# Kernel optimization log

Measured on AMD Instinct MI355X. Metric: run time of the kernel, lower is better.

## Reference

```python
import jax, jax.numpy as jnp
import numpy as np

EMBED_DIM = 768
NUM_HEADS = 12
HEAD_DIM = EMBED_DIM // NUM_HEADS
BSZ = 8
N_NODE = 512


def setup_inputs() -> dict:
    key = jax.random.key(0)
    ks = jax.random.split(key, 12)
    s = 0.02
    E = EMBED_DIM
    return {
        "query": jax.random.normal(ks[0], (N_NODE, BSZ, E), jnp.float32),
        "attention_bias": jax.random.normal(ks[1], (BSZ, NUM_HEADS, N_NODE, N_NODE), jnp.float32),
        "node_position": jax.random.normal(ks[2], (BSZ, N_NODE, 3), jnp.float32),
        "Wq": jax.random.normal(ks[3], (E, E), jnp.float32) * s,
        "bq": jnp.zeros((E,), jnp.float32),
        "Wk": jax.random.normal(ks[4], (E, E), jnp.float32) * s,
        "bk": jnp.zeros((E,), jnp.float32),
        "Wv": jax.random.normal(ks[5], (E, E), jnp.float32) * s,
        "bv": jnp.zeros((E,), jnp.float32),
        "W1": jax.random.normal(ks[6], (E, 1), jnp.float32) * s,
        "b1": jnp.zeros((1,), jnp.float32),
        "W2": jax.random.normal(ks[7], (E, 1), jnp.float32) * s,
        "b2": jnp.zeros((1,), jnp.float32),
        "W3": jax.random.normal(ks[8], (E, 1), jnp.float32) * s,
        "b3": jnp.zeros((1,), jnp.float32),
    }


def reference(query, attention_bias, node_position, Wq, bq, Wk, bk, Wv, bv,
              W1, b1, W2, b2, W3, b3):
    bsz, n = node_position.shape[:2]
    H = attention_bias.shape[1]
    E = query.shape[-1]
    hd = E // H
    scaling = hd ** -0.5

    # unit direction vectors between node pairs: delta[b,i,j] = pos[j]-pos[i]
    delta = node_position[:, None, :, :] - node_position[:, :, None, :]  # (b,n,n,3)
    dist = jnp.linalg.norm(delta, axis=-1)                               # (b,n,n)
    delta = delta / (dist[..., None] + 1e-5)

    x = jnp.swapaxes(query, 0, 1)  # (b,n,E)
    q = (x @ Wq + bq).reshape(bsz, n, H, hd).transpose(0, 2, 1, 3) * scaling  # (b,h,n,d)
    k = (x @ Wk + bk).reshape(bsz, n, H, hd).transpose(0, 2, 1, 3)
    v = (x @ Wv + bv).reshape(bsz, n, H, hd).transpose(0, 2, 1, 3)

    attn = jnp.einsum('bhid,bhjd->bhij', q, k)
    probs = jax.nn.softmax(attn + attention_bias, axis=-1)  # (b,h,i,j); dropout = identity (eval)

    # rotational aggregation: out[b,i,c,h,d] = sum_j probs[b,h,i,j]*delta[b,i,j,c]*v[b,h,j,d]
    xo = jnp.einsum('bhij,bijc,bhjd->bichd', probs, delta, v).reshape(bsz, n, 3, E)

    f1 = xo[:, :, 0, :] @ W1 + b1  # (b,n,1)
    f2 = xo[:, :, 1, :] @ W2 + b2
    f3 = xo[:, :, 2, :] @ W3 + b3
    return jnp.concatenate([f1, f2, f3], axis=-1).astype(jnp.float32)  # (b,n,3)
```

## Files before the change

kernel.cpp:

```cpp
#include <hip/hip_runtime.h>
#include <math.h>

#define EDIM 768
#define NH 12
#define HD 64
#define BSZ 8
#define NN 512
#define NCAT 1664

typedef short short8 __attribute__((ext_vector_type(8)));
typedef float f32x4 __attribute__((ext_vector_type(4)));

__device__ __forceinline__ unsigned short f2bf(float x) {
    unsigned int u = __float_as_uint(x);
    u = (u + 0x7FFF + ((u >> 16) & 1)) >> 16;
    return (unsigned short)u;
}
__device__ __forceinline__ void gl2lds16(const void* g, void* l) {
    __builtin_amdgcn_global_load_lds(
        (const __attribute__((address_space(1))) unsigned int*)g,
        (__attribute__((address_space(3))) unsigned int*)l, 16, 0, 0);
}

#define PB_TR_END   1152
#define PB_VW_END   1260
#define PB_CVT_END  2028
#define PB_BC_END   2035
#define PREP_BLOCKS 2070

__global__ __launch_bounds__(256) void k_prep(
        const float* __restrict__ query,
        const float* __restrict__ Wq, const float* __restrict__ bq,
        const float* __restrict__ Wk, const float* __restrict__ bk,
        const float* __restrict__ Wv, const float* __restrict__ bv,
        const float* __restrict__ W1, const float* __restrict__ W2,
        const float* __restrict__ W3,
        unsigned short* __restrict__ WT, float* __restrict__ bcat,
        unsigned short* __restrict__ Xb) {
    __shared__ float sm[1536];
    const int bid = blockIdx.x;
    const int t = threadIdx.x;

    if (bid < PB_TR_END) {
        float (*tile)[33] = (float(*)[33])sm;
        const int n0 = (bid % 48) * 32, e0 = (bid / 48) * 32;
        const float* src = (n0 < 768) ? Wq : Wk;
        const float sc = (n0 < 768) ? 0.125f : 1.0f;
        const int ol0 = (n0 < 768) ? n0 : (n0 - 768);
        const int tx = t & 31, ty = t >> 5;
        #pragma unroll
        for (int s = 0; s < 4; s++)
            tile[ty + s * 8][tx] = src[(size_t)(e0 + ty + s * 8) * EDIM + ol0 + tx];
        __syncthreads();
        #pragma unroll
        for (int s = 0; s < 4; s++)
            WT[(size_t)(n0 + ty + s * 8) * EDIM + e0 + tx] = f2bf(tile[tx][ty + s * 8] * sc);
    } else if (bid < PB_VW_END) {
        int idx = (bid - PB_TR_END) * 256 + t;
        int o2 = idx / 768, e = idx - o2 * 768;
        int h = o2 / 3, c = o2 - (o2 / 3) * 3;
        const float* Wc = (c == 0) ? W1 : (c == 1) ? W2 : W3;
        const float4* wvp = (const float4*)(Wv + (size_t)e * EDIM + h * HD);
        const float4* wcp = (const float4*)(Wc + h * HD);
        float s = 0.f;
        #pragma unroll
        for (int d4 = 0; d4 < 16; d4++) {
            float4 a = wvp[d4], b = wcp[d4];
            s += a.x * b.x + a.y * b.y + a.z * b.z + a.w * b.w;
        }
        WT[(size_t)(1536 + o2) * EDIM + e] = f2bf(s);
    } else if (bid < PB_CVT_END) {
        int base = (bid - PB_VW_END) * 256 + t;
        #pragma unroll
        for (int half = 0; half < 2; half++) {
            int idx = base + half * 196608;
            int m = idx / 96, e8 = (idx - (idx / 96) * 96) * 8;
            int b = m >> 9, i = m & (NN - 1);
            const float* src = query + ((size_t)i * BSZ + b) * EDIM + e8;
            float4 v0 = *(const float4*)src;
            float4 v1 = *(const float4*)(src + 4);
            unsigned int p0 = f2bf(v0.x) | ((unsigned int)f2bf(v0.y) << 16);
            unsigned int p1 = f2bf(v0.z) | ((unsigned int)f2bf(v0.w) << 16);
            unsigned int p2 = f2bf(v1.x) | ((unsigned int)f2bf(v1.y) << 16);
            unsigned int p3 = f2bf(v1.z) | ((unsigned int)f2bf(v1.w) << 16);
            uint4 pk = {p0, p1, p2, p3};
            *(uint4*)&Xb[(size_t)idx * 8] = pk;
        }
    } else if (bid < PB_BC_END) {
        int o = (bid - PB_CVT_END) * 256 + t;
        if (o < NCAT) {
            float v = 0.f;
            if (o < 768) v = bq[o] * 0.125f;
            else if (o < 1536) v = bk[o - 768];
            else if (o < 1572) {
                int o2 = o - 1536;
                int h = o2 / 3, c = o2 - (o2 / 3) * 3;
                const float* Wc = (c == 0) ? W1 : (c == 1) ? W2 : W3;
                float s = 0.f;
                for (int d = 0; d < HD; d++) s += bv[h * HD + d] * Wc[h * HD + d];
                v = s;
            }
            bcat[o] = v;
        }
    } else {
        int tid = (bid - PB_BC_END) * 256 + t;
        if (tid < 8832) {
            uint4 z = {0, 0, 0, 0};
            *(uint4*)&WT[(size_t)1572 * EDIM + (size_t)tid * 8] = z;
        }
    }
}

__global__ __launch_bounds__(256) void k_gemm_qkv(
        const unsigned short* __restrict__ Xb, const unsigned short* __restrict__ WT,
        const float* __restrict__ bcat,
        unsigned short* __restrict__ qb, unsigned short* __restrict__ kb,
        float* __restrict__ vwb) {
    __shared__ short As[8 * 128 * 8];
    __shared__ short Bs[8 * 128 * 8];
    const int t = threadIdx.x;
    const int m0 = blockIdx.x * 128, n0 = blockIdx.y * 128;
    const int w = t >> 6, lane = t & 63, quad = lane >> 4, ln = lane & 15;
    const int wr = (w & 1) * 64, wc = (w >> 1) * 64;

    f32x4 acc[4][4];
    #pragma unroll
    for (int mi = 0; mi < 4; mi++)
        #pragma unroll
        for (int ni = 0; ni < 4; ni++) acc[mi][ni] = (f32x4){0.f, 0.f, 0.f, 0.f};

    for (int k0 = 0; k0 < EDIM; k0 += 64) {
        __syncthreads();
        #pragma unroll
        for (int is = 0; is < 4; is++) {
            int slot = is * 256 + t;
            int g = slot >> 7, m = slot & 127;
            gl2lds16(Xb + (size_t)(m0 + m) * EDIM + k0 + g * 8, &As[(size_t)(is * 256 + w * 64) * 8]);
        }
        #pragma unroll
        for (int is = 0; is < 4; is++) {
            int slot = is * 256 + t;
            int g = slot >> 7, n = slot & 127;
            gl2lds16(WT + (size_t)(n0 + n) * EDIM + k0 + g * 8, &Bs[(size_t)(is * 256 + w * 64) * 8]);
        }
        __syncthreads();
        #pragma unroll
        for (int s = 0; s < 2; s++) {
            short8 af[4], bf[4];
            #pragma unroll
            for (int mi = 0; mi < 4; mi++)
                af[mi] = *(const short8*)&As[(size_t)((s * 4 + quad) * 128 + wr + mi * 16 + ln) * 8];
            #pragma unroll
            for (int ni = 0; ni < 4; ni++)
                bf[ni] = *(const short8*)&Bs[(size_t)((s * 4 + quad) * 128 + wc + ni * 16 + ln) * 8];
            #pragma unroll
            for (int mi = 0; mi < 4; mi++)
                #pragma unroll
                for (int ni = 0; ni < 4; ni++)
                    acc[mi][ni] = __builtin_amdgcn_mfma_f32_16x16x32_bf16(af[mi], bf[ni], acc[mi][ni], 0, 0, 0);
        }
    }

    #pragma unroll
    for (int mi = 0; mi < 4; mi++) {
        #pragma unroll
        for (int r = 0; r < 4; r++) {
            int mg = m0 + wr + mi * 16 + quad * 4 + r;
            int b_ = mg >> 9, i_ = mg & (NN - 1);
            #pragma unroll
            for (int ni = 0; ni < 4; ni++) {
                int o = n0 + wc + ni * 16 + ln;
                float val = acc[mi][ni][r] + bcat[o];
                if (o < 768) {
                    int h = o >> 6, d = o & 63;
                    qb[(((size_t)b_ * NH + h) * NN + i_) * HD + d] = f2bf(val);
                } else if (o < 1536) {
                    int o2 = o - 768;
                    int h = o2 >> 6, d = o2 & 63;
                    kb[(((size_t)b_ * NH + h) * NN + i_) * HD + d] = f2bf(val);
                } else if (o < 1572) {
                    int o2 = o - 1536;
                    int h = o2 / 3, c = o2 - (o2 / 3) * 3;
                    vwb[(((size_t)b_ * NH + h) * NN + i_) * 3 + c] = val;
                }
            }
        }
    }
}

__global__ __launch_bounds__(256, 6) void k_attn(
        const unsigned short* __restrict__ qb, const unsigned short* __restrict__ kb,
        const float* __restrict__ vwb, const float* __restrict__ bias,
        const float* __restrict__ pos,
        float* __restrict__ mp, float* __restrict__ lp,
        float* __restrict__ a0p, float* __restrict__ a1p, float* __restrict__ a2p) {
    __shared__ uint4 Ks[128 * 8];
    __shared__ float ws0[128], ws1[128], ws2[128];
    __shared__ float pjx[128], pjy[128], pjz[128];
    __shared__ float pix[64], piy[64], piz[64];

    const int t = threadIdx.x;
    const int bid = blockIdx.x;
    const int h = bid % NH;
    const int r1 = bid / NH;
    const int js = r1 & 3;
    const int it = (r1 >> 2) & 7;
    const int b = r1 >> 5;
    const int i0 = it * 64;
    const int jb = js * 128;
    const int w = t >> 6, lane = t & 63, quad = lane >> 4, ln = lane & 15;
    const size_t bh = (size_t)b * NH + h;

    const uint4* kg = (const uint4*)(kb + (bh * NN + jb) * HD);
    const int rr = t >> 3, cc = t & 7;
    uint4 kv0 = kg[t];
    uint4 kv1 = kg[256 + t];
    uint4 kv2 = kg[512 + t];
    uint4 kv3 = kg[768 + t];
    float wv0 = vwb[bh * (NN * 3) + (size_t)jb * 3 + t];
    float wv1 = (t < 128) ? vwb[bh * (NN * 3) + (size_t)jb * 3 + 256 + t] : 0.f;

    const unsigned short* qrow = qb + (bh * NN + i0 + w * 16 + ln) * HD;
    short8 a0f = *(const short8*)(qrow + quad * 8);
    short8 a1f = *(const short8*)(qrow + 32 + quad * 8);

    const float* bbase = bias + (bh * NN + i0 + w * 16 + quad * 4) * NN + jb + ln;
    f32x4 acc[8];
    #pragma unroll
    for (int jsub = 0; jsub < 8; jsub++)
        #pragma unroll
        for (int r = 0; r < 4; r++)
            acc[jsub][r] = bbase[r * NN + jsub * 16];

    for (int idx = t; idx < 384; idx += 256) {
        float pv = pos[((size_t)b * NN + jb) * 3 + idx];
        int jj = idx / 3, c = idx - (idx / 3) * 3;
        if (c == 0) pjx[jj] = pv; else if (c == 1) pjy[jj] = pv; else pjz[jj] = pv;
    }
    if (t < 192) {
        float pv = pos[((size_t)b * NN + i0) * 3 + t];
        int ii = t / 3, c = t - (t / 3) * 3;
        if (c == 0) pix[ii] = pv; else if (c == 1) piy[ii] = pv; else piz[ii] = pv;
    }

    const int sw = cc ^ (rr & 7);
    Ks[rr * 8 + sw] = kv0;
    Ks[(rr + 32) * 8 + sw] = kv1;
    Ks[(rr + 64) * 8 + sw] = kv2;
    Ks[(rr + 96) * 8 + sw] = kv3;
    {
        int jj = t / 3, c = t - (t / 3) * 3;
        if (c == 0) ws0[jj] = wv0; else if (c == 1) ws1[jj] = wv0; else ws2[jj] = wv0;
        if (t < 128) {
            int t2 = 256 + t;
            int jj2 = t2 / 3, c2 = t2 - (t2 / 3) * 3;
            if (c2 == 0) ws0[jj2] = wv1; else if (c2 == 1) ws1[jj2] = wv1; else ws2[jj2] = wv1;
        }
    }
    __syncthreads();

    #pragma unroll
    for (int jsub = 0; jsub < 8; jsub++) {
        int krow = jsub * 16 + ln;
        short8 b0f = *(const short8*)&Ks[krow * 8 + (quad ^ (krow & 7))];
        short8 b1f = *(const short8*)&Ks[krow * 8 + ((quad + 4) ^ (krow & 7))];
        acc[jsub] = __builtin_amdgcn_mfma_f32_16x16x32_bf16(a0f, b0f, acc[jsub], 0, 0, 0);
        acc[jsub] = __builtin_amdgcn_mfma_f32_16x16x32_bf16(a1f, b1f, acc[jsub], 0, 0, 0);
    }

    float m_r = acc[0][0];
    #pragma unroll
    for (int jsub = 0; jsub < 8; jsub++)
        #pragma unroll
        for (int r = 0; r < 4; r++) m_r = fmaxf(m_r, acc[jsub][r]);
    #pragma unroll
    for (int off = 1; off < 64; off <<= 1) m_r = fmaxf(m_r, __shfl_xor(m_r, off, 64));

    const int irbase = w * 16 + quad * 4;
    float lr[4] = {0.f, 0.f, 0.f, 0.f};
    float A0[4] = {0.f, 0.f, 0.f, 0.f};
    float A1[4] = {0.f, 0.f, 0.f, 0.f};
    float A2[4] = {0.f, 0.f, 0.f, 0.f};
    #pragma unroll
    for (int jsub = 0; jsub < 8; jsub++) {
        const int jl = jsub * 16 + ln;
        float w0 = ws0[jl], w1 = ws1[jl], w2 = ws2[jl];
        float px = pjx[jl], py = pjy[jl], pz = pjz[jl];
        #pragma unroll
        for (int r = 0; r < 4; r++) {
            float dx = px - pix[irbase + r];
            float dy = py - piy[irbase + r];
            float dz = pz - piz[irbase + r];
            float d2 = fmaf(dx, dx, fmaf(dy, dy, dz * dz));
            float inv = __builtin_amdgcn_rcpf(__builtin_amdgcn_sqrtf(d2) + 1e-5f);
            float p = __expf(acc[jsub][r] - m_r);
            float pi = p * inv;
            lr[r] += p;
            A0[r] = fmaf(pi * dx, w0, A0[r]);
            A1[r] = fmaf(pi * dy, w1, A1[r]);
            A2[r] = fmaf(pi * dz, w2, A2[r]);
        }
    }

    #pragma unroll
    for (int off = 1; off < 16; off <<= 1) {
        #pragma unroll
        for (int r = 0; r < 4; r++) {
            lr[r] += __shfl_xor(lr[r], off, 64);
            A0[r] += __shfl_xor(A0[r], off, 64);
            A1[r] += __shfl_xor(A1[r], off, 64);
            A2[r] += __shfl_xor(A2[r], off, 64);
        }
    }
    if (ln == 0) {
        #pragma unroll
        for (int r = 0; r < 4; r++) {
            int ig = i0 + irbase + r;
            size_t o4 = (bh * NN + ig) * 4 + js;
            mp[o4] = m_r; lp[o4] = lr[r];
            a0p[o4] = A0[r]; a1p[o4] = A1[r]; a2p[o4] = A2[r];
        }
    }
}

__global__ __launch_bounds__(256) void k_finalize(
        const float* __restrict__ mp, const float* __restrict__ lp,
        const float* __restrict__ a0p, const float* __restrict__ a1p,
        const float* __restrict__ a2p,
        const float* __restrict__ b1, const float* __restrict__ b2,
        const float* __restrict__ b3, float* __restrict__ out) {
    __shared__ float red[NH][16][3];
    const int t = threadIdx.x;
    const int g0 = blockIdx.x * 16;
    const int b = g0 >> 9;
    const int i0 = g0 & (NN - 1);

    if (t < NH * 16) {
        int h = t >> 4, row = t & 15;
        size_t base = (((size_t)b * NH + h) * NN + i0 + row) * 4;
        f32x4 mv = *(const f32x4*)&mp[base];
        f32x4 lv = *(const f32x4*)&lp[base];
        f32x4 A0 = *(const f32x4*)&a0p[base];
        f32x4 A1 = *(const f32x4*)&a1p[base];
        f32x4 A2 = *(const f32x4*)&a2p[base];
        float M = fmaxf(fmaxf(mv[0], mv[1]), fmaxf(mv[2], mv[3]));
        float L = 0.f, c0 = 0.f, c1 = 0.f, c2 = 0.f;
        #pragma unroll
        for (int js = 0; js < 4; js++) {
            float e = __expf(mv[js] - M);
            L = fmaf(e, lv[js], L);
            c0 = fmaf(e, A0[js], c0);
            c1 = fmaf(e, A1[js], c1);
            c2 = fmaf(e, A2[js], c2);
        }
        float inv = 1.f / L;
        red[h][row][0] = c0 * inv;
        red[h][row][1] = c1 * inv;
        red[h][row][2] = c2 * inv;
    }
    __syncthreads();
    if (t < 48) {
        int row = t / 3, c = t - row * 3;
        float s = 0.f;
        #pragma unroll
        for (int h = 0; h < NH; h++) s += red[h][row][c];
        const float* bb = (c == 0) ? b1 : (c == 1) ? b2 : b3;
        out[((size_t)g0 + row) * 3 + c] = s + bb[0];
    }
}

extern "C" void kernel_launch(void* const* d_in, const int* in_sizes, int n_in,
                              void* d_out, int out_size, void* d_ws, size_t ws_size,
                              hipStream_t stream) {
    const float* query = (const float*)d_in[0];
    const float* bias  = (const float*)d_in[1];
    const float* pos   = (const float*)d_in[2];
    const float* Wq = (const float*)d_in[3];
    const float* bq = (const float*)d_in[4];
    const float* Wk = (const float*)d_in[5];
    const float* bk = (const float*)d_in[6];
    const float* Wv = (const float*)d_in[7];
    const float* bv = (const float*)d_in[8];
    const float* W1 = (const float*)d_in[9];
    const float* b1 = (const float*)d_in[10];
    const float* W2 = (const float*)d_in[11];
    const float* b2 = (const float*)d_in[12];
    const float* W3 = (const float*)d_in[13];
    const float* b3 = (const float*)d_in[14];
    float* out = (float*)d_out;

    char* p = (char*)d_ws;
    unsigned short* WT = (unsigned short*)p; p += (size_t)NCAT * EDIM * 2;
    float* bcat = (float*)p;                 p += (size_t)NCAT * 4;
    unsigned short* Xb = (unsigned short*)p; p += (size_t)BSZ * NN * EDIM * 2;
    unsigned short* qb = (unsigned short*)p; p += (size_t)BSZ * NH * NN * HD * 2;
    unsigned short* kb = (unsigned short*)p; p += (size_t)BSZ * NH * NN * HD * 2;
    float* vwb = (float*)p;                  p += (size_t)BSZ * NH * NN * 3 * 4;
    const size_t PSZ = (size_t)BSZ * NH * NN * 4;
    float* mp  = (float*)p; p += PSZ * 4;
    float* lp  = (float*)p; p += PSZ * 4;
    float* a0p = (float*)p; p += PSZ * 4;
    float* a1p = (float*)p; p += PSZ * 4;
    float* a2p = (float*)p; p += PSZ * 4;

    k_prep<<<PREP_BLOCKS, 256, 0, stream>>>(query, Wq, bq, Wk, bk, Wv, bv,
                                            W1, W2, W3, WT, bcat, Xb);
    dim3 g2(32, 13);
    k_gemm_qkv<<<g2, 256, 0, stream>>>(Xb, WT, bcat, qb, kb, vwb);
    k_attn<<<BSZ * NH * 8 * 4, 256, 0, stream>>>(qb, kb, vwb, bias, pos,
                                                 mp, lp, a0p, a1p, a2p);
    k_finalize<<<BSZ * NN / 16, 256, 0, stream>>>(mp, lp, a0p, a1p, a2p, b1, b2, b3, out);
}
```

Before: 239.5 us.

## Loop over key tiles inside attention block with online softmax, drop split-K partials

The attention kernel no longer splits the key dimension across four blocks. Each block now walks all four 128-key tiles with an online-softmax rescale, loading K tiles straight into LDS via global_load_lds. It writes normalized per-head outputs, so finalize becomes a simple per-output sum over heads. This removes the partial m/l/A buffers and the cross-block merge. In exchange the grid shrinks fourfold (768 blocks), parallelism drops, and there is no double buffering, so load latency inside the loop may be exposed.

After: 276.8 us. 15.6% more time.

```diff
diff --git a/kernel.cpp b/kernel.cpp
--- a/kernel.cpp
+++ b/kernel.cpp
@@ -188,125 +188,133 @@
     }
 }
 
-__global__ __launch_bounds__(256, 6) void k_attn(
+__global__ __launch_bounds__(256, 3) void k_attn(
         const unsigned short* __restrict__ qb, const unsigned short* __restrict__ kb,
         const float* __restrict__ vwb, const float* __restrict__ bias,
-        const float* __restrict__ pos,
-        float* __restrict__ mp, float* __restrict__ lp,
-        float* __restrict__ a0p, float* __restrict__ a1p, float* __restrict__ a2p) {
+        const float* __restrict__ pos, float* __restrict__ co) {
     __shared__ uint4 Ks[128 * 8];
     __shared__ float ws0[128], ws1[128], ws2[128];
     __shared__ float pjx[128], pjy[128], pjz[128];
     __shared__ float pix[64], piy[64], piz[64];
 
     const int t = threadIdx.x;
-    const int bid = blockIdx.x;
-    const int h = bid % NH;
-    const int r1 = bid / NH;
-    const int js = r1 & 3;
-    const int it = (r1 >> 2) & 7;
-    const int b = r1 >> 5;
+    const int bid = (blockIdx.x & 7) * 96 + (blockIdx.x >> 3);
+    const int it = bid & 7;
+    const int h = (bid >> 3) % NH;
+    const int b = bid / 96;
     const int i0 = it * 64;
-    const int jb = js * 128;
     const int w = t >> 6, lane = t & 63, quad = lane >> 4, ln = lane & 15;
     const size_t bh = (size_t)b * NH + h;
 
-    const uint4* kg = (const uint4*)(kb + (bh * NN + jb) * HD);
-    const int rr = t >> 3, cc = t & 7;
-    uint4 kv0 = kg[t];
-    uint4 kv1 = kg[256 + t];
-    uint4 kv2 = kg[512 + t];
-    uint4 kv3 = kg[768 + t];
-    float wv0 = vwb[bh * (NN * 3) + (size_t)jb * 3 + t];
-    float wv1 = (t < 128) ? vwb[bh * (NN * 3) + (size_t)jb * 3 + 256 + t] : 0.f;
-
-    const unsigned short* qrow = qb + (bh * NN + i0 + w * 16 + ln) * HD;
-    short8 a0f = *(const short8*)(qrow + quad * 8);
-    short8 a1f = *(const short8*)(qrow + 32 + quad * 8);
-
-    const float* bbase = bias + (bh * NN + i0 + w * 16 + quad * 4) * NN + jb + ln;
-    f32x4 acc[8];
-    #pragma unroll
-    for (int jsub = 0; jsub < 8; jsub++)
-        #pragma unroll
-        for (int r = 0; r < 4; r++)
-            acc[jsub][r] = bbase[r * NN + jsub * 16];
-
-    for (int idx = t; idx < 384; idx += 256) {
-        float pv = pos[((size_t)b * NN + jb) * 3 + idx];
-        int jj = idx / 3, c = idx - (idx / 3) * 3;
-        if (c == 0) pjx[jj] = pv; else if (c == 1) pjy[jj] = pv; else pjz[jj] = pv;
-    }
     if (t < 192) {
         float pv = pos[((size_t)b * NN + i0) * 3 + t];
         int ii = t / 3, c = t - (t / 3) * 3;
         if (c == 0) pix[ii] = pv; else if (c == 1) piy[ii] = pv; else piz[ii] = pv;
     }
 
-    const int sw = cc ^ (rr & 7);
-    Ks[rr * 8 + sw] = kv0;
-    Ks[(rr + 32) * 8 + sw] = kv1;
-    Ks[(rr + 64) * 8 + sw] = kv2;
-    Ks[(rr + 96) * 8 + sw] = kv3;
-    {
-        int jj = t / 3, c = t - (t / 3) * 3;
-        if (c == 0) ws0[jj] = wv0; else if (c == 1) ws1[jj] = wv0; else ws2[jj] = wv0;
-        if (t < 128) {
-            int t2 = 256 + t;
-            int jj2 = t2 / 3, c2 = t2 - (t2 / 3) * 3;
-            if (c2 == 0) ws0[jj2] = wv1; else if (c2 == 1) ws1[jj2] = wv1; else ws2[jj2] = wv1;
-        }
-    }
-    __syncthreads();
-
-    #pragma unroll
-    for (int jsub = 0; jsub < 8; jsub++) {
-        int krow = jsub * 16 + ln;
-        short8 b0f = *(const short8*)&Ks[krow * 8 + (quad ^ (krow & 7))];
-        short8 b1f = *(const short8*)&Ks[krow * 8 + ((quad + 4) ^ (krow & 7))];
-        acc[jsub] = __builtin_amdgcn_mfma_f32_16x16x32_bf16(a0f, b0f, acc[jsub], 0, 0, 0);
-        acc[jsub] = __builtin_amdgcn_mfma_f32_16x16x32_bf16(a1f, b1f, acc[jsub], 0, 0, 0);
-    }
-
-    float m_r = acc[0][0];
-    #pragma unroll
-    for (int jsub = 0; jsub < 8; jsub++)
-        #pragma unroll
-        for (int r = 0; r < 4; r++) m_r = fmaxf(m_r, acc[jsub][r]);
-    #pragma unroll
-    for (int off = 1; off < 64; off <<= 1) m_r = fmaxf(m_r, __shfl_xor(m_r, off, 64));
+    const unsigned short* qrow = qb + (bh * NN + i0 + w * 16 + ln) * HD;
+    short8 a0f = *(const short8*)(qrow + quad * 8);
+    short8 a1f = *(const short8*)(qrow + 32 + quad * 8);
 
     const int irbase = w * 16 + quad * 4;
-    float lr[4] = {0.f, 0.f, 0.f, 0.f};
+    float M = -1e30f;
+    float L[4]  = {0.f, 0.f, 0.f, 0.f};
     float A0[4] = {0.f, 0.f, 0.f, 0.f};
     float A1[4] = {0.f, 0.f, 0.f, 0.f};
     float A2[4] = {0.f, 0.f, 0.f, 0.f};
-    #pragma unroll
-    for (int jsub = 0; jsub < 8; jsub++) {
-        const int jl = jsub * 16 + ln;
-        float w0 = ws0[jl], w1 = ws1[jl], w2 = ws2[jl];
-        float px = pjx[jl], py = pjy[jl], pz = pjz[jl];
-        #pragma unroll
-        for (int r = 0; r < 4; r++) {
-            float dx = px - pix[irbase + r];
-            float dy = py - piy[irbase + r];
-            float dz = pz - piz[irbase + r];
-            float d2 = fmaf(dx, dx, fmaf(dy, dy, dz * dz));
-            float inv = __builtin_amdgcn_rcpf(__builtin_amdgcn_sqrtf(d2) + 1e-5f);
-            float p = __expf(acc[jsub][r] - m_r);
-            float pi = p * inv;
-            lr[r] += p;
-            A0[r] = fmaf(pi * dx, w0, A0[r]);
-            A1[r] = fmaf(pi * dy, w1, A1[r]);
-            A2[r] = fmaf(pi * dz, w2, A2[r]);
-        }
+
+    const char* kbase = (const char*)(kb + bh * NN * HD);
+
+    for (int js = 0; js < 4; js++) {
+        const int jb = js * 128;
+
+        #pragma unroll
+        for (int is = 0; is < 4; is++) {
+            int unit = is * 256 + w * 64 + lane;
+            int rl = unit >> 3, cc = unit & 7;
+            const char* src = kbase + (size_t)(jb + rl) * 128 + ((cc ^ (rl & 7)) << 4);
+            gl2lds16(src, &Ks[is * 256 + w * 64]);
+        }
+
+        {
+            const float* vwt = vwb + bh * (NN * 3) + (size_t)jb * 3;
+            float wv0 = vwt[t];
+            int jj = t / 3, c = t - (t / 3) * 3;
+            if (c == 0) ws0[jj] = wv0; else if (c == 1) ws1[jj] = wv0; else ws2[jj] = wv0;
+            if (t < 128) {
+                float wv1 = vwt[256 + t];
+                int t2 = 256 + t;
+                int jj2 = t2 / 3, c2 = t2 - (t2 / 3) * 3;
+                if (c2 == 0) ws0[jj2] = wv1; else if (c2 == 1) ws1[jj2] = wv1; else ws2[jj2] = wv1;
+            }
+            for (int idx = t; idx < 384; idx += 256) {
+                float pv = pos[((size_t)b * NN + jb) * 3 + idx];
+                int jjp = idx / 3, cp = idx - (idx / 3) * 3;
+                if (cp == 0) pjx[jjp] = pv; else if (cp == 1) pjy[jjp] = pv; else pjz[jjp] = pv;
+            }
+        }
+
+        const float* bbase = bias + (bh * NN + i0 + w * 16 + quad * 4) * NN + jb + ln;
+        f32x4 acc[8];
+        #pragma unroll
+        for (int jsub = 0; jsub < 8; jsub++)
+            #pragma unroll
+            for (int r = 0; r < 4; r++)
+                acc[jsub][r] = bbase[r * NN + jsub * 16];
+
+        __syncthreads();
+
+        #pragma unroll
+        for (int jsub = 0; jsub < 8; jsub++) {
+            int krow = jsub * 16 + ln;
+            short8 b0f = *(const short8*)&Ks[krow * 8 + (quad ^ (krow & 7))];
+            short8 b1f = *(const short8*)&Ks[krow * 8 + ((quad + 4) ^ (krow & 7))];
+            acc[jsub] = __builtin_amdgcn_mfma_f32_16x16x32_bf16(a0f, b0f, acc[jsub], 0, 0, 0);
+            acc[jsub] = __builtin_amdgcn_mfma_f32_16x16x32_bf16(a1f, b1f, acc[jsub], 0, 0, 0);
+        }
+
+        float m_t = acc[0][0];
+        #pragma unroll
+        for (int jsub = 0; jsub < 8; jsub++)
+            #pragma unroll
+            for (int r = 0; r < 4; r++) m_t = fmaxf(m_t, acc[jsub][r]);
+        #pragma unroll
+        for (int off = 1; off < 64; off <<= 1) m_t = fmaxf(m_t, __shfl_xor(m_t, off, 64));
+
+        float newM = fmaxf(M, m_t);
+        float sc = __expf(M - newM);
+        #pragma unroll
+        for (int r = 0; r < 4; r++) { L[r] *= sc; A0[r] *= sc; A1[r] *= sc; A2[r] *= sc; }
+        M = newM;
+
+        #pragma unroll
+        for (int jsub = 0; jsub < 8; jsub++) {
+            const int jl = jsub * 16 + ln;
+            float w0 = ws0[jl], w1 = ws1[jl], w2 = ws2[jl];
+            float px = pjx[jl], py = pjy[jl], pz = pjz[jl];
+            #pragma unroll
+            for (int r = 0; r < 4; r++) {
+                float dx = px - pix[irbase + r];
+                float dy = py - piy[irbase + r];
+                float dz = pz - piz[irbase + r];
+                float d2 = fmaf(dx, dx, fmaf(dy, dy, dz * dz));
+                float inv = __builtin_amdgcn_rcpf(__builtin_amdgcn_sqrtf(d2) + 1e-5f);
+                float p = __expf(acc[jsub][r] - M);
+                float pi = p * inv;
+                L[r] += p;
+                A0[r] = fmaf(pi * dx, w0, A0[r]);
+                A1[r] = fmaf(pi * dy, w1, A1[r]);
+                A2[r] = fmaf(pi * dz, w2, A2[r]);
+            }
+        }
+        __syncthreads();
     }
 
     #pragma unroll
     for (int off = 1; off < 16; off <<= 1) {
         #pragma unroll
         for (int r = 0; r < 4; r++) {
-            lr[r] += __shfl_xor(lr[r], off, 64);
+            L[r]  += __shfl_xor(L[r],  off, 64);
             A0[r] += __shfl_xor(A0[r], off, 64);
             A1[r] += __shfl_xor(A1[r], off, 64);
             A2[r] += __shfl_xor(A2[r], off, 64);
@@ -316,57 +324,28 @@
         #pragma unroll
         for (int r = 0; r < 4; r++) {
             int ig = i0 + irbase + r;
-            size_t o4 = (bh * NN + ig) * 4 + js;
-            mp[o4] = m_r; lp[o4] = lr[r];
-            a0p[o4] = A0[r]; a1p[o4] = A1[r]; a2p[o4] = A2[r];
+            float inv = 1.f / L[r];
+            size_t base = (size_t)((b * NN + ig) * 3) * NH + h;
+            co[base + 0 * NH] = A0[r] * inv;
+            co[base + 1 * NH] = A1[r] * inv;
+            co[base + 2 * NH] = A2[r] * inv;
         }
     }
 }
 
 __global__ __launch_bounds__(256) void k_finalize(
-        const float* __restrict__ mp, const float* __restrict__ lp,
-        const float* __restrict__ a0p, const float* __restrict__ a1p,
-        const float* __restrict__ a2p,
+        const float* __restrict__ co,
         const float* __restrict__ b1, const float* __restrict__ b2,
         const float* __restrict__ b3, float* __restrict__ out) {
-    __shared__ float red[NH][16][3];
-    const int t = threadIdx.x;
-    const int g0 = blockIdx.x * 16;
-    const int b = g0 >> 9;
-    const int i0 = g0 & (NN - 1);
-
-    if (t < NH * 16) {
-        int h = t >> 4, row = t & 15;
-        size_t base = (((size_t)b * NH + h) * NN + i0 + row) * 4;
-        f32x4 mv = *(const f32x4*)&mp[base];
-        f32x4 lv = *(const f32x4*)&lp[base];
-        f32x4 A0 = *(const f32x4*)&a0p[base];
-        f32x4 A1 = *(const f32x4*)&a1p[base];
-        f32x4 A2 = *(const f32x4*)&a2p[base];
-        float M = fmaxf(fmaxf(mv[0], mv[1]), fmaxf(mv[2], mv[3]));
-        float L = 0.f, c0 = 0.f, c1 = 0.f, c2 = 0.f;
-        #pragma unroll
-        for (int js = 0; js < 4; js++) {
-            float e = __expf(mv[js] - M);
-            L = fmaf(e, lv[js], L);
-            c0 = fmaf(e, A0[js], c0);
-            c1 = fmaf(e, A1[js], c1);
-            c2 = fmaf(e, A2[js], c2);
-        }
-        float inv = 1.f / L;
-        red[h][row][0] = c0 * inv;
-        red[h][row][1] = c1 * inv;
-        red[h][row][2] = c2 * inv;
-    }
-    __syncthreads();
-    if (t < 48) {
-        int row = t / 3, c = t - row * 3;
-        float s = 0.f;
-        #pragma unroll
-        for (int h = 0; h < NH; h++) s += red[h][row][c];
-        const float* bb = (c == 0) ? b1 : (c == 1) ? b2 : b3;
-        out[((size_t)g0 + row) * 3 + c] = s + bb[0];
-    }
+    int idx = blockIdx.x * 256 + threadIdx.x;
+    const f32x4* p = (const f32x4*)(co + (size_t)idx * NH);
+    f32x4 v0 = p[0], v1 = p[1], v2 = p[2];
+    float s = (v0[0] + v0[1] + v0[2] + v0[3])
+            + (v1[0] + v1[1] + v1[2] + v1[3])
+            + (v2[0] + v2[1] + v2[2] + v2[3]);
+    int c = idx - (idx / 3) * 3;
+    const float* bb = (c == 0) ? b1 : (c == 1) ? b2 : b3;
+    out[idx] = s + bb[0];
 }
 
 extern "C" void kernel_launch(void* const* d_in, const int* in_sizes, int n_in,
@@ -396,18 +375,12 @@
     unsigned short* qb = (unsigned short*)p; p += (size_t)BSZ * NH * NN * HD * 2;
     unsigned short* kb = (unsigned short*)p; p += (size_t)BSZ * NH * NN * HD * 2;
     float* vwb = (float*)p;                  p += (size_t)BSZ * NH * NN * 3 * 4;
-    const size_t PSZ = (size_t)BSZ * NH * NN * 4;
-    float* mp  = (float*)p; p += PSZ * 4;
-    float* lp  = (float*)p; p += PSZ * 4;
-    float* a0p = (float*)p; p += PSZ * 4;
-    float* a1p = (float*)p; p += PSZ * 4;
-    float* a2p = (float*)p; p += PSZ * 4;
+    float* co  = (float*)p;                  p += (size_t)BSZ * NN * 3 * NH * 4;
 
     k_prep<<<PREP_BLOCKS, 256, 0, stream>>>(query, Wq, bq, Wk, bk, Wv, bv,
                                             W1, W2, W3, WT, bcat, Xb);
     dim3 g2(32, 13);
     k_gemm_qkv<<<g2, 256, 0, stream>>>(Xb, WT, bcat, qb, kb, vwb);
-    k_attn<<<BSZ * NH * 8 * 4, 256, 0, stream>>>(qb, kb, vwb, bias, pos,
-                                                 mp, lp, a0p, a1p, a2p);
-    k_finalize<<<BSZ * NN / 16, 256, 0, stream>>>(mp, lp, a0p, a1p, a2p, b1, b2, b3, out);
-}
+    k_attn<<<BSZ * NH * 8, 256, 0, stream>>>(qb, kb, vwb, bias, pos, co);
+    k_finalize<<<BSZ * NN * 3 / 256, 256, 0, stream>>>(co, b1, b2, b3, out);
+}
```
